# Performance work log

Measured on AMD Instinct MI355X. Metric: run time of the kernel, lower is better.

## Reference

```python
import jax, jax.numpy as jnp
import numpy as np

N_NODES = 100000
N_EDGES = 1000000
N_GRAPHS = 64
NODE_IN = 4
HID = 64
SIG = 16
NEG_SLOPE = 0.2


def _gat_layer(x, src, dst, W, a_src, a_dst, bias, n_nodes, concat):
    # W: [H*D, F_in], a_src/a_dst: [H, D], bias: [H*D] or [D]
    H, D = a_src.shape
    h = (x @ W.T).reshape(-1, H, D)                      # [N, H, D]
    alpha_src = jnp.sum(h * a_src[None], axis=-1)        # [N, H]
    alpha_dst = jnp.sum(h * a_dst[None], axis=-1)        # [N, H]
    e = alpha_src[src] + alpha_dst[dst]                  # [E, H]
    e = jax.nn.leaky_relu(e, NEG_SLOPE)
    # segment softmax over edges grouped by destination node
    e_max = jax.ops.segment_max(e, dst, num_segments=n_nodes)   # [N, H]
    e_exp = jnp.exp(e - e_max[dst])                              # [E, H]
    denom = jax.ops.segment_sum(e_exp, dst, num_segments=n_nodes)
    alpha = e_exp / denom[dst]                                   # [E, H]
    out = jax.ops.segment_sum(alpha[:, :, None] * h[src], dst, num_segments=n_nodes)  # [N,H,D]
    if concat:
        out = out.reshape(-1, H * D)
    else:
        out = out.mean(axis=1)
    return out + bias


def setup_inputs() -> dict:
    key = jax.random.key(0)
    ks = jax.random.split(key, 16)
    x = jax.random.normal(ks[0], (N_NODES, NODE_IN), dtype=jnp.float32)
    edge_index = jax.random.randint(ks[1], (2, N_EDGES), 0, N_NODES, dtype=jnp.int32)
    batch = jnp.sort(jax.random.randint(ks[2], (N_NODES,), 0, N_GRAPHS, dtype=jnp.int32))
    s = 0.1
    # conv1: heads=2, concat -> out 128
    w1 = jax.random.normal(ks[3], (2 * HID, NODE_IN), dtype=jnp.float32) * s
    att_src1 = jax.random.normal(ks[4], (2, HID), dtype=jnp.float32) * s
    att_dst1 = jax.random.normal(ks[5], (2, HID), dtype=jnp.float32) * s
    b1 = jnp.zeros((2 * HID,), dtype=jnp.float32)
    # conv2: heads=1, mean -> out 64
    w2 = jax.random.normal(ks[6], (HID, 2 * HID), dtype=jnp.float32) * s
    att_src2 = jax.random.normal(ks[7], (1, HID), dtype=jnp.float32) * s
    att_dst2 = jax.random.normal(ks[8], (1, HID), dtype=jnp.float32) * s
    b2 = jnp.zeros((HID,), dtype=jnp.float32)
    wp = jax.random.normal(ks[9], (SIG, HID), dtype=jnp.float32) * s
    bp = jnp.zeros((SIG,), dtype=jnp.float32)
    return {"x": x, "edge_index": edge_index, "batch": batch,
            "w1": w1, "att_src1": att_src1, "att_dst1": att_dst1, "b1": b1,
            "w2": w2, "att_src2": att_src2, "att_dst2": att_dst2, "b2": b2,
            "wp": wp, "bp": bp}


def reference(x, edge_index, batch, w1, att_src1, att_dst1, b1,
              w2, att_src2, att_dst2, b2, wp, bp):
    n = x.shape[0]
    loops = jnp.arange(n, dtype=edge_index.dtype)
    src = jnp.concatenate([edge_index[0], loops])  # PyG GATConv adds self-loops
    dst = jnp.concatenate([edge_index[1], loops])
    h = jax.nn.elu(_gat_layer(x, src, dst, w1, att_src1, att_dst1, b1, n, concat=True))
    h = jax.nn.elu(_gat_layer(h, src, dst, w2, att_src2, att_dst2, b2, n, concat=False))
    # global mean pool by graph id
    sums = jax.ops.segment_sum(h, batch, num_segments=N_GRAPHS)
    cnts = jax.ops.segment_sum(jnp.ones((n,), h.dtype), batch, num_segments=N_GRAPHS)
    pooled = sums / jnp.maximum(cnts, 1.0)[:, None]
    return (pooled @ wp.T + bp).squeeze()
```

## Files before the change

kernel.cpp:

```cpp
#include <hip/hip_runtime.h>
#include <hip/hip_fp16.h>

#define N_NODES  100000
#define N_EDGES  1000000
#define E_TOT    1100000
#define E_CAP    1900000
#define N_GRAPHS 64

#define BSH    9
#define BSIZE  512
#define NBUCK  ((N_NODES + BSIZE - 1) / BSIZE)
#define CHUNK  4096
#define NBLKS  ((E_TOT + CHUNK - 1) / CHUNK)

typedef _Float16 half8 __attribute__((ext_vector_type(8)));
typedef float    f32x4 __attribute__((ext_vector_type(4)));

__device__ __forceinline__ float elu_f(float v) {
    return v > 0.f ? v : expm1f(v);
}

__device__ __forceinline__ float lrelu(float v) {
    return v > 0.f ? v : 0.2f * v;
}

__global__ void k_preall(const float* __restrict__ w1,
                         const float* __restrict__ as1v, const float* __restrict__ ad1v,
                         const float* __restrict__ w2,
                         const float* __restrict__ as2v, const float* __restrict__ ad2v,
                         float* __restrict__ A1, float* __restrict__ D1,
                         float* __restrict__ B2, float* __restrict__ E2,
                         __half* __restrict__ w2frag)
{
    if (blockIdx.x == 0) {
        int t = threadIdx.x;
        if (t < 128) {
            float acc = 0.f;
            for (int d = 0; d < 64; ++d) acc += w2[d * 128 + t] * as2v[d];
            B2[t] = acc;
        } else {
            int k = t - 128;
            float acc = 0.f;
            for (int d = 0; d < 64; ++d) acc += w2[d * 128 + k] * ad2v[d];
            E2[k] = acc;
        }
        if (t < 8) {
            int h = t >> 2, k = t & 3;
            float acc = 0.f;
            for (int d = 0; d < 64; ++d) acc += w1[(h * 64 + d) * 4 + k] * as1v[h * 64 + d];
            A1[t] = acc;
        } else if (t < 16) {
            int i = t - 8, h = i >> 2, k = i & 3;
            float acc = 0.f;
            for (int d = 0; d < 64; ++d) acc += w1[(h * 64 + d) * 4 + k] * ad1v[h * 64 + d];
            D1[i] = acc;
        }
    } else {
        int f = (blockIdx.x - 1) * 256 + threadIdx.x;
        int j = f & 7, ln = (f >> 3) & 63, g = f >> 9;
        int nt = g >> 2, ks = g & 3;
        int col = nt * 16 + (ln & 15);
        int k   = ks * 32 + ((ln >> 4) << 3) + j;
        w2frag[f] = __float2half(w2[col * 128 + k]);
    }
}

__global__ void __launch_bounds__(256) k_bin1(
    const int* __restrict__ ei, int* __restrict__ bucketCount, int* __restrict__ blockoff)
{
    __shared__ int hist[NBUCK];
    const int t = threadIdx.x;
    for (int i = t; i < NBUCK; i += 256) hist[i] = 0;
    __syncthreads();
    const int e0 = blockIdx.x * CHUNK;
    for (int i = t; i < CHUNK; i += 256) {
        int e = e0 + i;
        if (e < E_TOT) {
            int dst = (e < N_EDGES) ? ei[N_EDGES + e] : (e - N_EDGES);
            atomicAdd(&hist[dst >> BSH], 1);
        }
    }
    __syncthreads();
    for (int i = t; i < NBUCK; i += 256)
        blockoff[blockIdx.x * NBUCK + i] = atomicAdd(&bucketCount[i], hist[i]);
}

__global__ void k_bscan(const int* __restrict__ bucketCount, int* __restrict__ bucketStart)
{
    __shared__ int sh[256];
    int t = threadIdx.x;
    int v = (t < NBUCK) ? bucketCount[t] : 0;
    int acc = v;
    sh[t] = acc; __syncthreads();
    for (int off = 1; off < 256; off <<= 1) {
        int add = (t >= off) ? sh[t - off] : 0;
        __syncthreads();
        acc += add; sh[t] = acc; __syncthreads();
    }
    if (t < NBUCK) bucketStart[t] = acc - v;
}

__global__ void __launch_bounds__(256) k_bin2(
    const int* __restrict__ ei, const int* __restrict__ bucketStart,
    const int* __restrict__ blockoff, unsigned int* __restrict__ bucketed)
{
    __shared__ int cur[NBUCK];
    const int t = threadIdx.x;
    for (int i = t; i < NBUCK; i += 256)
        cur[i] = bucketStart[i] + blockoff[blockIdx.x * NBUCK + i];
    __syncthreads();
    const int e0 = blockIdx.x * CHUNK;
    for (int i = t; i < CHUNK; i += 256) {
        int e = e0 + i;
        if (e < E_TOT) {
            int src = (e < N_EDGES) ? ei[e] : (e - N_EDGES);
            int dst = (e < N_EDGES) ? ei[N_EDGES + e] : (e - N_EDGES);
            int b = dst >> BSH;
            int p = atomicAdd(&cur[b], 1);
            bucketed[p] = (unsigned)src | ((unsigned)(dst & (BSIZE - 1)) << 17);
        }
    }
}

__global__ void __launch_bounds__(256) k_bhist(
    const unsigned int* __restrict__ bucketed,
    const int* __restrict__ bucketStart, const int* __restrict__ bucketCount,
    int* __restrict__ deg, int* __restrict__ rowptr, int* __restrict__ bucketPad)
{
    __shared__ int hist[BSIZE];
    __shared__ int sh[256];
    const int t = threadIdx.x;
    const int b = blockIdx.x;
    hist[t] = 0; hist[t + 256] = 0;
    __syncthreads();
    const int beg = bucketStart[b], cnt = bucketCount[b];
    for (int i = t; i < cnt; i += 256)
        atomicAdd(&hist[bucketed[beg + i] >> 17], 1);
    __syncthreads();
    int h0 = hist[2 * t], h1 = hist[2 * t + 1];
    int a = (h0 + 7) & ~7, c = (h1 + 7) & ~7;
    int s = a + c;
    sh[t] = s; __syncthreads();
    for (int off = 1; off < 256; off <<= 1) {
        int add = (t >= off) ? sh[t - off] : 0;
        __syncthreads();
        s += add; sh[t] = s; __syncthreads();
    }
    int base = s - a - c;
    const int n0 = b * BSIZE;
    int na = n0 + 2 * t, nb = n0 + 2 * t + 1;
    if (na < N_NODES) { deg[na] = h0; rowptr[na] = base; }
    if (nb < N_NODES) { deg[nb] = h1; rowptr[nb] = base + a; }
    if (t == 255) bucketPad[b] = s;
}

__global__ void k_bscan2(const int* __restrict__ bucketPad, int* __restrict__ bucketBase,
                         int* __restrict__ rowptr)
{
    __shared__ int sh[256];
    int t = threadIdx.x;
    int v = (t < NBUCK) ? bucketPad[t] : 0;
    int acc = v;
    sh[t] = acc; __syncthreads();
    for (int off = 1; off < 256; off <<= 1) {
        int add = (t >= off) ? sh[t - off] : 0;
        __syncthreads();
        acc += add; sh[t] = acc; __syncthreads();
    }
    if (t < NBUCK) bucketBase[t] = acc - v;
    if (t == NBUCK - 1) rowptr[N_NODES] = acc;
}

__global__ void __launch_bounds__(256) k_bscat(
    const unsigned int* __restrict__ bucketed,
    const int* __restrict__ bucketStart, const int* __restrict__ bucketCount,
    const int* __restrict__ bucketBase, int* __restrict__ rowptr, int* __restrict__ srcs)
{
    __shared__ int cur[BSIZE];
    const int t = threadIdx.x;
    const int b = blockIdx.x;
    const int base = bucketBase[b];
    const int n0 = b * BSIZE;
    #pragma unroll
    for (int k = 0; k < 2; ++k) {
        int nl = t + k * 256;
        int n = n0 + nl;
        if (n < N_NODES) {
            int r = rowptr[n] + base;
            rowptr[n] = r;
            cur[nl] = r;
        }
    }
    __syncthreads();
    const int beg = bucketStart[b], cnt = bucketCount[b];
    for (int i = t; i < cnt; i += 256) {
        unsigned p = bucketed[beg + i];
        int rank = atomicAdd(&cur[p >> 17], 1);
        srcs[rank] = (int)(p & 0x1FFFFu);
    }
}

__global__ void __launch_bounds__(256) k_gather1x(
    const int* __restrict__ srcs, const int* __restrict__ rowptr, const int* __restrict__ deg,
    const float* __restrict__ x,
    const float* __restrict__ A1c, const float* __restrict__ D1c,
    float4* __restrict__ agg0, float4* __restrict__ agg1, float2* __restrict__ wsA)
{
    const int tid  = threadIdx.x;
    const int n    = blockIdx.x * 16 + (tid >> 4);
    const int lane = tid & 15;
    if (n >= N_NODES) return;

    const float4 A0 = ((const float4*)A1c)[0], A1v = ((const float4*)A1c)[1];
    const float4 D0 = ((const float4*)D1c)[0], D1v = ((const float4*)D1c)[1];
    const float4 xn = ((const float4*)x)[n];
    const float ad0 = xn.x * D0.x + xn.y * D0.y + xn.z * D0.z + xn.w * D0.w;
    const float ad1 = xn.x * D1v.x + xn.y * D1v.y + xn.z * D1v.z + xn.w * D1v.w;

    const int beg = rowptr[n], rend = beg + deg[n];
    float4 acc0 = {0.f, 0.f, 0.f, 0.f}, acc1 = {0.f, 0.f, 0.f, 0.f};
    float ws0 = 0.f, ws1 = 0.f;
    for (int j = beg + lane; j < rend; j += 16) {
        const int s = srcs[j];
        const float4 xs = ((const float4*)x)[s];
        const float as0 = xs.x * A0.x + xs.y * A0.y + xs.z * A0.z + xs.w * A0.w;
        const float as1 = xs.x * A1v.x + xs.y * A1v.y + xs.z * A1v.z + xs.w * A1v.w;
        const float w0 = __expf(lrelu(as0 + ad0));
        const float w1 = __expf(lrelu(as1 + ad1));
        acc0.x = fmaf(w0, xs.x, acc0.x); acc0.y = fmaf(w0, xs.y, acc0.y);
        acc0.z = fmaf(w0, xs.z, acc0.z); acc0.w = fmaf(w0, xs.w, acc0.w);
        acc1.x = fmaf(w1, xs.x, acc1.x); acc1.y = fmaf(w1, xs.y, acc1.y);
        acc1.z = fmaf(w1, xs.z, acc1.z); acc1.w = fmaf(w1, xs.w, acc1.w);
        ws0 += w0; ws1 += w1;
    }
    #pragma unroll
    for (int off = 1; off < 16; off <<= 1) {
        acc0.x += __shfl_xor(acc0.x, off, 64);
        acc0.y += __shfl_xor(acc0.y, off, 64);
        acc0.z += __shfl_xor(acc0.z, off, 64);
        acc0.w += __shfl_xor(acc0.w, off, 64);
        acc1.x += __shfl_xor(acc1.x, off, 64);
        acc1.y += __shfl_xor(acc1.y, off, 64);
        acc1.z += __shfl_xor(acc1.z, off, 64);
        acc1.w += __shfl_xor(acc1.w, off, 64);
        ws0    += __shfl_xor(ws0,    off, 64);
        ws1    += __shfl_xor(ws1,    off, 64);
    }
    if (lane == 0) {
        agg0[n] = acc0;
        agg1[n] = acc1;
        wsA[n]  = make_float2(ws0, ws1);
    }
}

#define H2_NPB 64
#define SROW_H_LD 136
__global__ void __launch_bounds__(256) k_h2f(
    const float4* __restrict__ agg0, const float4* __restrict__ agg1,
    const float2* __restrict__ wsA,
    const float* __restrict__ w1, const float* __restrict__ b1,
    const __half* __restrict__ w2frag,
    const float* __restrict__ B2, const float* __restrict__ E2,
    __half* __restrict__ h2h, float* __restrict__ as2, float* __restrict__ ad2)
{
    __shared__ __align__(16) _Float16 srow[H2_NPB * SROW_H_LD];
    const int tid = threadIdx.x;
    const int bn  = blockIdx.x * H2_NPB;

    #pragma unroll 4
    for (int t = 0; t < 16; ++t) {
        int i = tid + t * 256;
        int r = i >> 6, c2 = i & 63;
        int n = bn + r;
        int head = c2 >> 5;
        float4 a; float ws;
        if (n < N_NODES) {
            a = head ? agg1[n] : agg0[n];
            float2 w = wsA[n];
            ws = head ? w.y : w.x;
        } else { a = make_float4(0.f, 0.f, 0.f, 0.f); ws = 1.f; }
        const float4 wA = ((const float4*)w1)[2 * c2];
        const float4 wB = ((const float4*)w1)[2 * c2 + 1];
        const float2 bb = ((const float2*)b1)[c2];
        float inv = 1.f / ws;
        float v0 = elu_f((a.x * wA.x + a.y * wA.y + a.z * wA.z + a.w * wA.w) * inv + bb.x);
        float v1 = elu_f((a.x * wB.x + a.y * wB.y + a.z * wB.z + a.w * wB.w) * inv + bb.y);
        *(__half2*)&srow[r * SROW_H_LD + 2 * c2] = __floats2half2_rn(v0, v1);
    }
    __syncthreads();

    {
        int r = tid >> 2, q = tid & 3;
        const __half2* row = (const __half2*)&srow[r * SROW_H_LD];
        float ps = 0.f, pd = 0.f;
        #pragma unroll 4
        for (int i = 0; i < 16; ++i) {
            int c2 = q * 16 + i;
            float2 v  = __half22float2(row[c2]);
            float2 Bv = ((const float2*)B2)[c2];
            float2 Ev = ((const float2*)E2)[c2];
            ps += v.x * Bv.x + v.y * Bv.y;
            pd += v.x * Ev.x + v.y * Ev.y;
        }
        ps += __shfl_xor(ps, 1, 64); ps += __shfl_xor(ps, 2, 64);
        pd += __shfl_xor(pd, 1, 64); pd += __shfl_xor(pd, 2, 64);
        int n = bn + r;
        if (q == 0 && n < N_NODES) { as2[n] = ps; ad2[n] = pd; }
    }

    const int lane = tid & 63;
    const int wv   = tid >> 6;
    const int mrow = lane & 15;
    const int kc   = lane >> 4;
    f32x4 acc[4] = {{0.f,0.f,0.f,0.f},{0.f,0.f,0.f,0.f},{0.f,0.f,0.f,0.f},{0.f,0.f,0.f,0.f}};
    const half8* __restrict__ wf = (const half8*)w2frag;
    #pragma unroll
    for (int ks = 0; ks < 4; ++ks) {
        const half8 af = *(const half8*)&srow[(wv * 16 + mrow) * SROW_H_LD + ks * 32 + kc * 8];
        #pragma unroll
        for (int nt = 0; nt < 4; ++nt) {
            const half8 bf = wf[(nt * 4 + ks) * 64 + lane];
            acc[nt] = __builtin_amdgcn_mfma_f32_16x16x32_f16(af, bf, acc[nt], 0, 0, 0);
        }
    }
    #pragma unroll
    for (int nt = 0; nt < 4; ++nt) {
        #pragma unroll
        for (int reg = 0; reg < 4; ++reg) {
            int node = bn + wv * 16 + ((lane >> 4) << 2) + reg;
            int dim  = nt * 16 + (lane & 15);
            if (node < N_NODES) h2h[(size_t)node * 64 + dim] = __float2half(acc[nt][reg]);
        }
    }
}

__global__ void __launch_bounds__(256) k_weights2(
    const int* __restrict__ rowptr, const int* __restrict__ deg, int* __restrict__ srcs,
    const float* __restrict__ as2, const float* __restrict__ ad2,
    float* __restrict__ w0p)
{
    int n = blockIdx.x * 16 + (threadIdx.x >> 4);
    int lane = threadIdx.x & 15;
    if (n >= N_NODES) return;
    int beg = rowptr[n], pend = rowptr[n + 1], rend = beg + deg[n];
    float adv = ad2[n];
    for (int j = beg + lane; j < pend; j += 16) {
        if (j < rend) {
            w0p[j] = __expf(lrelu(as2[srcs[j]] + adv));
        } else {
            srcs[j] = 0;
            w0p[j] = 0.f;
        }
    }
}

__global__ void __launch_bounds__(256) k_gather2(
    const int* __restrict__ srcs, const int* __restrict__ rowptr,
    const float* __restrict__ wcsr, const _Float16* __restrict__ h2h,
    const float* __restrict__ b2, float* __restrict__ out2, int nbase)
{
    const int tid  = threadIdx.x;
    const int n    = nbase + blockIdx.x * 4 + (tid >> 6);
    const int lane = tid & 63;
    const int eg   = lane >> 3;
    const int dq   = lane & 7;
    const int beg = rowptr[n], end = rowptr[n + 1];

    half8 hacc = {0, 0, 0, 0, 0, 0, 0, 0};
    float wsum = 0.f;
    for (int j = beg + eg; j < end; j += 8) {
        const int   s = srcs[j];
        const float w = wcsr[j];
        const half8 v = *(const half8*)&h2h[(size_t)s * 64 + dq * 8];
        const _Float16 wh = (_Float16)w;
        const half8 ws8 = {wh, wh, wh, wh, wh, wh, wh, wh};
        hacc += v * ws8;
        wsum += w;
    }
    float a0 = (float)hacc[0], a1 = (float)hacc[1], a2 = (float)hacc[2], a3 = (float)hacc[3];
    float a4 = (float)hacc[4], a5 = (float)hacc[5], a6 = (float)hacc[6], a7 = (float)hacc[7];
    #pragma unroll
    for (int off = 8; off < 64; off <<= 1) {
        a0 += __shfl_xor(a0, off, 64);
        a1 += __shfl_xor(a1, off, 64);
        a2 += __shfl_xor(a2, off, 64);
        a3 += __shfl_xor(a3, off, 64);
        a4 += __shfl_xor(a4, off, 64);
        a5 += __shfl_xor(a5, off, 64);
        a6 += __shfl_xor(a6, off, 64);
        a7 += __shfl_xor(a7, off, 64);
        wsum += __shfl_xor(wsum, off, 64);
    }
    if (eg == 0) {
        const float inv = 1.f / wsum;
        const float4 bA = ((const float4*)b2)[dq * 2];
        const float4 bB = ((const float4*)b2)[dq * 2 + 1];
        float4 oA, oB;
        oA.x = elu_f(a0 * inv + bA.x);
        oA.y = elu_f(a1 * inv + bA.y);
        oA.z = elu_f(a2 * inv + bA.z);
        oA.w = elu_f(a3 * inv + bA.w);
        oB.x = elu_f(a4 * inv + bB.x);
        oB.y = elu_f(a5 * inv + bB.y);
        oB.z = elu_f(a6 * inv + bB.z);
        oB.w = elu_f(a7 * inv + bB.w);
        float4* orow = (float4*)(out2 + (size_t)n * 64);
        orow[dq * 2]     = oA;
        orow[dq * 2 + 1] = oB;
    }
}

__global__ void __launch_bounds__(256) k_pool(
    const float* __restrict__ out2, const int* __restrict__ batch,
    float* __restrict__ pool, float* __restrict__ cnt)
{
    const int wv = threadIdx.x >> 6, d = threadIdx.x & 63;
    const int wid = blockIdx.x * 4 + wv;
    const int per = (N_NODES + 2047) / 2048;
    int n0 = wid * per, n1 = min(n0 + per, N_NODES);
    if (n0 >= n1) return;
    float acc = 0.f; int g = batch[n0]; int run = 0;
    for (int n = n0; n < n1; ++n) {
        int gn = batch[n];
        if (gn != g) {
            atomicAdd(&pool[g * 64 + d], acc);
            if (d == 0) atomicAdd(&cnt[g], (float)run);
            acc = 0.f; run = 0; g = gn;
        }
        acc += out2[(size_t)n * 64 + d];
        ++run;
    }
    atomicAdd(&pool[g * 64 + d], acc);
    if (d == 0) atomicAdd(&cnt[g], (float)run);
}

__global__ void k_head(const float* __restrict__ pool, const float* __restrict__ cnt,
                       const float* __restrict__ wp, const float* __restrict__ bp,
                       float* __restrict__ out)
{
    int t = threadIdx.x;
    int g = t >> 4, s = t & 15;
    float c = cnt[g]; if (c < 1.f) c = 1.f;
    float acc = bp[s];
    for (int d = 0; d < 64; ++d) acc += (pool[g * 64 + d] / c) * wp[s * 64 + d];
    out[g * 16 + s] = acc;
}

extern "C" void kernel_launch(void* const* d_in, const int* in_sizes, int n_in,
                              void* d_out, int out_size, void* d_ws, size_t ws_size,
                              hipStream_t stream)
{
    const float* x     = (const float*)d_in[0];
    const int*   ei    = (const int*)  d_in[1];
    const int*   batch = (const int*)  d_in[2];
    const float* w1    = (const float*)d_in[3];
    const float* asr1  = (const float*)d_in[4];
    const float* adr1  = (const float*)d_in[5];
    const float* b1    = (const float*)d_in[6];
    const float* w2    = (const float*)d_in[7];
    const float* asr2  = (const float*)d_in[8];
    const float* adr2  = (const float*)d_in[9];
    const float* b2    = (const float*)d_in[10];
    const float* wp    = (const float*)d_in[11];
    const float* bp    = (const float*)d_in[12];
    float* out = (float*)d_out;

    float4* agg0 = (float4*)d_ws;
    float4* agg1 = agg0 + N_NODES;
    float2* wsA  = (float2*)(agg1 + N_NODES);
    __half* h2h  = (__half*)(wsA + N_NODES);
    float* out2  = (float*)(h2h + (size_t)N_NODES * 64);
    float* as2   = out2 + (size_t)N_NODES * 64;
    float* ad2   = as2 + N_NODES;
    float* pool  = ad2 + N_NODES;
    float* cnt   = pool + N_GRAPHS * 64;
    int* deg     = (int*)(cnt + N_GRAPHS);
    int* rowptr  = deg + N_NODES;
    unsigned int* bucketed = (unsigned int*)(rowptr + N_NODES + 1);
    int* srcs    = (int*)(bucketed + E_TOT);
    float* wcsr  = (float*)(srcs + E_CAP);
    int* blockoff    = (int*)(wcsr + E_CAP);
    int* bucketCount = blockoff + NBLKS * NBUCK;
    int* bucketStart = bucketCount + NBUCK;
    int* bucketPad   = bucketStart + NBUCK;
    int* bucketBase  = bucketPad + NBUCK;
    float* A1    = (float*)(bucketBase + NBUCK);
    float* D1    = A1 + 8;
    float* B2    = D1 + 8;
    float* E2    = B2 + 128;
    __half* w2frag = (__half*)(((uintptr_t)(E2 + 128) + 15) & ~(uintptr_t)15);

    hipMemsetAsync(bucketCount, 0, NBUCK * sizeof(int), stream);
    hipMemsetAsync(pool, 0, (size_t)(N_GRAPHS * 64 + N_GRAPHS) * sizeof(float), stream);

    k_preall<<<33, 256, 0, stream>>>(w1, asr1, adr1, w2, asr2, adr2, A1, D1, B2, E2, w2frag);

    k_bin1 <<<NBLKS, 256, 0, stream>>>(ei, bucketCount, blockoff);
    k_bscan<<<1, 256, 0, stream>>>(bucketCount, bucketStart);
    k_bin2 <<<NBLKS, 256, 0, stream>>>(ei, bucketStart, blockoff, bucketed);
    k_bhist<<<NBUCK, 256, 0, stream>>>(bucketed, bucketStart, bucketCount, deg, rowptr, bucketPad);
    k_bscan2<<<1, 256, 0, stream>>>(bucketPad, bucketBase, rowptr);
    k_bscat<<<NBUCK, 256, 0, stream>>>(bucketed, bucketStart, bucketCount, bucketBase, rowptr, srcs);

    const int gb = (N_NODES + 15) / 16;
    k_gather1x<<<gb, 256, 0, stream>>>(srcs, rowptr, deg, x, A1, D1, agg0, agg1, wsA);

    k_h2f<<<(N_NODES + H2_NPB - 1) / H2_NPB, 256, 0, stream>>>(
        agg0, agg1, wsA, w1, b1, w2frag, B2, E2, h2h, as2, ad2);

    k_weights2<<<gb, 256, 0, stream>>>(rowptr, deg, srcs, as2, ad2, wcsr);
    k_gather2<<<N_NODES / 8, 256, 0, stream>>>(srcs, rowptr, wcsr, (const _Float16*)h2h,
                                               b2, out2, 0);
    k_gather2<<<N_NODES / 8, 256, 0, stream>>>(srcs, rowptr, wcsr, (const _Float16*)h2h,
                                               b2, out2, N_NODES / 2);

    k_pool<<<512, 256, 0, stream>>>(out2, batch, pool, cnt);
    k_head<<<1, 1024, 0, stream>>>(pool, cnt, wp, bp, out);
}
```

Measured before the change: 215.0 us.

## Fuse layer-2 edge weight computation into gather and fold memsets into preprocessing

Removes the separate k_weights2 pass and its wcsr array; the layer-2 gather now computes exp(leaky_relu(as2[s]+ad2[n])) inline per edge, using -1 sentinels for padded CSR slots, which k_bscat now writes. The two half-size gather2 launches become one, and the two hipMemsetAsync calls are replaced by zeroing inside k_preall. This saves a full edge pass of writes and reads plus several launches, at the cost of an extra random as2 load in the gather and sentinel writes in the scatter.

Measured after the change: 197.5 us. -8.2%, faster.

```diff
diff --git a/kernel.cpp b/kernel.cpp
--- a/kernel.cpp
+++ b/kernel.cpp
@@ -30,7 +30,8 @@
                          const float* __restrict__ as2v, const float* __restrict__ ad2v,
                          float* __restrict__ A1, float* __restrict__ D1,
                          float* __restrict__ B2, float* __restrict__ E2,
-                         __half* __restrict__ w2frag)
+                         __half* __restrict__ w2frag,
+                         int* __restrict__ bucketCount, float* __restrict__ poolcnt)
 {
     if (blockIdx.x == 0) {
         int t = threadIdx.x;
@@ -55,6 +56,7 @@
             for (int d = 0; d < 64; ++d) acc += w1[(h * 64 + d) * 4 + k] * ad1v[h * 64 + d];
             D1[i] = acc;
         }
+        if (t < NBUCK) bucketCount[t] = 0;
     } else {
         int f = (blockIdx.x - 1) * 256 + threadIdx.x;
         int j = f & 7, ln = (f >> 3) & 63, g = f >> 9;
@@ -62,6 +64,8 @@
         int col = nt * 16 + (ln & 15);
         int k   = ks * 32 + ((ln >> 4) << 3) + j;
         w2frag[f] = __float2half(w2[col * 128 + k]);
+        int z = (blockIdx.x - 1) * 256 + threadIdx.x;
+        if (z < N_GRAPHS * 64 + N_GRAPHS) poolcnt[z] = 0.f;
     }
 }
 
@@ -174,7 +178,8 @@
 __global__ void __launch_bounds__(256) k_bscat(
     const unsigned int* __restrict__ bucketed,
     const int* __restrict__ bucketStart, const int* __restrict__ bucketCount,
-    const int* __restrict__ bucketBase, int* __restrict__ rowptr, int* __restrict__ srcs)
+    const int* __restrict__ bucketBase, const int* __restrict__ bucketPad,
+    int* __restrict__ rowptr, int* __restrict__ srcs)
 {
     __shared__ int cur[BSIZE];
     const int t = threadIdx.x;
@@ -197,6 +202,17 @@
         unsigned p = bucketed[beg + i];
         int rank = atomicAdd(&cur[p >> 17], 1);
         srcs[rank] = (int)(p & 0x1FFFFu);
+    }
+    __syncthreads();
+    const int bend = base + bucketPad[b];
+    #pragma unroll
+    for (int k = 0; k < 2; ++k) {
+        int nl = t + k * 256;
+        int n = n0 + nl;
+        if (n < N_NODES) {
+            int e = (nl == BSIZE - 1 || n == N_NODES - 1) ? bend : rowptr[n + 1];
+            for (int j = cur[nl]; j < e; ++j) srcs[j] = -1;
+        }
     }
 }
 
@@ -334,44 +350,28 @@
     }
 }
 
-__global__ void __launch_bounds__(256) k_weights2(
-    const int* __restrict__ rowptr, const int* __restrict__ deg, int* __restrict__ srcs,
-    const float* __restrict__ as2, const float* __restrict__ ad2,
-    float* __restrict__ w0p)
-{
-    int n = blockIdx.x * 16 + (threadIdx.x >> 4);
-    int lane = threadIdx.x & 15;
-    if (n >= N_NODES) return;
-    int beg = rowptr[n], pend = rowptr[n + 1], rend = beg + deg[n];
-    float adv = ad2[n];
-    for (int j = beg + lane; j < pend; j += 16) {
-        if (j < rend) {
-            w0p[j] = __expf(lrelu(as2[srcs[j]] + adv));
-        } else {
-            srcs[j] = 0;
-            w0p[j] = 0.f;
-        }
-    }
-}
-
 __global__ void __launch_bounds__(256) k_gather2(
     const int* __restrict__ srcs, const int* __restrict__ rowptr,
-    const float* __restrict__ wcsr, const _Float16* __restrict__ h2h,
-    const float* __restrict__ b2, float* __restrict__ out2, int nbase)
+    const float* __restrict__ as2, const float* __restrict__ ad2,
+    const _Float16* __restrict__ h2h, const float* __restrict__ b2,
+    float* __restrict__ out2)
 {
     const int tid  = threadIdx.x;
-    const int n    = nbase + blockIdx.x * 4 + (tid >> 6);
+    const int n    = blockIdx.x * 4 + (tid >> 6);
     const int lane = tid & 63;
     const int eg   = lane >> 3;
     const int dq   = lane & 7;
     const int beg = rowptr[n], end = rowptr[n + 1];
+    const float adv = ad2[n];
 
     half8 hacc = {0, 0, 0, 0, 0, 0, 0, 0};
     float wsum = 0.f;
     for (int j = beg + eg; j < end; j += 8) {
-        const int   s = srcs[j];
-        const float w = wcsr[j];
-        const half8 v = *(const half8*)&h2h[(size_t)s * 64 + dq * 8];
+        const int s = srcs[j];
+        const int sa = (s >= 0) ? s : 0;
+        float w = 0.f;
+        if (s >= 0) w = __expf(lrelu(as2[s] + adv));
+        const half8 v = *(const half8*)&h2h[(size_t)sa * 64 + dq * 8];
         const _Float16 wh = (_Float16)w;
         const half8 ws8 = {wh, wh, wh, wh, wh, wh, wh, wh};
         hacc += v * ws8;
@@ -478,8 +478,7 @@
     int* rowptr  = deg + N_NODES;
     unsigned int* bucketed = (unsigned int*)(rowptr + N_NODES + 1);
     int* srcs    = (int*)(bucketed + E_TOT);
-    float* wcsr  = (float*)(srcs + E_CAP);
-    int* blockoff    = (int*)(wcsr + E_CAP);
+    int* blockoff    = srcs + E_CAP;
     int* bucketCount = blockoff + NBLKS * NBUCK;
     int* bucketStart = bucketCount + NBUCK;
     int* bucketPad   = bucketStart + NBUCK;
@@ -490,17 +489,16 @@
     float* E2    = B2 + 128;
     __half* w2frag = (__half*)(((uintptr_t)(E2 + 128) + 15) & ~(uintptr_t)15);
 
-    hipMemsetAsync(bucketCount, 0, NBUCK * sizeof(int), stream);
-    hipMemsetAsync(pool, 0, (size_t)(N_GRAPHS * 64 + N_GRAPHS) * sizeof(float), stream);
-
-    k_preall<<<33, 256, 0, stream>>>(w1, asr1, adr1, w2, asr2, adr2, A1, D1, B2, E2, w2frag);
+    k_preall<<<33, 256, 0, stream>>>(w1, asr1, adr1, w2, asr2, adr2,
+                                     A1, D1, B2, E2, w2frag, bucketCount, pool);
 
     k_bin1 <<<NBLKS, 256, 0, stream>>>(ei, bucketCount, blockoff);
     k_bscan<<<1, 256, 0, stream>>>(bucketCount, bucketStart);
     k_bin2 <<<NBLKS, 256, 0, stream>>>(ei, bucketStart, blockoff, bucketed);
     k_bhist<<<NBUCK, 256, 0, stream>>>(bucketed, bucketStart, bucketCount, deg, rowptr, bucketPad);
     k_bscan2<<<1, 256, 0, stream>>>(bucketPad, bucketBase, rowptr);
-    k_bscat<<<NBUCK, 256, 0, stream>>>(bucketed, bucketStart, bucketCount, bucketBase, rowptr, srcs);
+    k_bscat<<<NBUCK, 256, 0, stream>>>(bucketed, bucketStart, bucketCount, bucketBase,
+                                       bucketPad, rowptr, srcs);
 
     const int gb = (N_NODES + 15) / 16;
     k_gather1x<<<gb, 256, 0, stream>>>(srcs, rowptr, deg, x, A1, D1, agg0, agg1, wsA);
@@ -508,11 +506,8 @@
     k_h2f<<<(N_NODES + H2_NPB - 1) / H2_NPB, 256, 0, stream>>>(
         agg0, agg1, wsA, w1, b1, w2frag, B2, E2, h2h, as2, ad2);
 
-    k_weights2<<<gb, 256, 0, stream>>>(rowptr, deg, srcs, as2, ad2, wcsr);
-    k_gather2<<<N_NODES / 8, 256, 0, stream>>>(srcs, rowptr, wcsr, (const _Float16*)h2h,
-                                               b2, out2, 0);
-    k_gather2<<<N_NODES / 8, 256, 0, stream>>>(srcs, rowptr, wcsr, (const _Float16*)h2h,
-                                               b2, out2, N_NODES / 2);
+    k_gather2<<<N_NODES / 4, 256, 0, stream>>>(srcs, rowptr, as2, ad2,
+                                               (const _Float16*)h2h, b2, out2);
 
     k_pool<<<512, 256, 0, stream>>>(out2, batch, pool, cnt);
     k_head<<<1, 1024, 0, stream>>>(pool, cnt, wp, bp, out);
```
